# Kernel tuning notes

Measured on AMD Instinct MI355X. Metric: run time of the kernel, lower is better.

Reference implementation:

```python
import jax, jax.numpy as jnp
import numpy as np

B, T, D, H = 8, 1024, 1024, 16
HD = D // H
SCALE = HD ** -0.5


def setup_inputs() -> dict:
    key = jax.random.key(0)
    ks = jax.random.split(key, 5)
    s = 0.02
    return {
        "hidden_states": jax.random.normal(ks[0], (B, T, D), jnp.float32),
        "Wq": jax.random.normal(ks[1], (D, D), jnp.float32) * s,
        "bq": jnp.zeros((D,), jnp.float32),
        "Wk": jax.random.normal(ks[2], (D, D), jnp.float32) * s,
        "bk": jnp.zeros((D,), jnp.float32),
        "Wv": jax.random.normal(ks[3], (D, D), jnp.float32) * s,
        "bv": jnp.zeros((D,), jnp.float32),
        "Wo": jax.random.normal(ks[4], (D, D), jnp.float32) * s,
        "bo": jnp.zeros((D,), jnp.float32),
    }


def _split_heads(x):
    # [B, T, D] -> [B, H, T, HD]
    return x.reshape(B, T, H, HD).transpose(0, 2, 1, 3)


def reference(hidden_states, Wq, bq, Wk, bk, Wv, bv, Wo, bo):
    q = _split_heads((hidden_states @ Wq + bq) * SCALE)
    k = _split_heads(hidden_states @ Wk + bk)
    v = _split_heads(hidden_states @ Wv + bv)
    # [B, H, T, T] attention scores
    scores = jnp.einsum("bhqd,bhkd->bhqk", q, k)
    probs = jax.nn.softmax(scores, axis=-1)
    attn = jnp.einsum("bhqk,bhkd->bhqd", probs, v)
    attn = attn.transpose(0, 2, 1, 3).reshape(B, T, D)
    return attn @ Wo + bo
```

## Files before the change

kernel.cpp:

```cpp
#include <hip/hip_runtime.h>

typedef unsigned short u16;
typedef __attribute__((ext_vector_type(4))) float f32x4;
typedef __attribute__((ext_vector_type(8))) __bf16 bf16x8;
typedef __attribute__((ext_vector_type(4))) __bf16 bf16x4;
typedef __attribute__((ext_vector_type(4))) unsigned short u16x4;
typedef __attribute__((ext_vector_type(8))) unsigned short u16x8;

static __device__ __forceinline__ u16 f2bf(float f) {
    union { float f; unsigned u; } v; v.f = f;
    unsigned r = v.u + 0x7FFFu + ((v.u >> 16) & 1u);
    return (u16)(r >> 16);
}

static __device__ __forceinline__ float exp2f_fast(float x) {
    float r; asm("v_exp_f32 %0, %1" : "=v"(r) : "v"(x)); return r;
}

static __device__ __forceinline__ void gload16(const u16* g, u16* l) {
    __builtin_amdgcn_global_load_lds(
        (const __attribute__((address_space(1))) unsigned int*)g,
        (__attribute__((address_space(3))) unsigned int*)l, 16, 0, 0);
}

template<int N> static __device__ __forceinline__ void vm_wait() {
    if constexpr (N >= 8)      asm volatile("s_waitcnt vmcnt(8)" ::: "memory");
    else if constexpr (N == 6) asm volatile("s_waitcnt vmcnt(6)" ::: "memory");
    else if constexpr (N == 4) asm volatile("s_waitcnt vmcnt(4)" ::: "memory");
    else if constexpr (N == 3) asm volatile("s_waitcnt vmcnt(3)" ::: "memory");
    else                       asm volatile("s_waitcnt vmcnt(0)" ::: "memory");
}

#define SWZ64(row, ec) (((row) * 64) + ((((ec) ^ ((row) & 7))) << 3))

__global__ __launch_bounds__(256) void k_cvt(const float* __restrict__ in, u16* __restrict__ out) {
    size_t i = (size_t)blockIdx.x * 256 + threadIdx.x;
    float4 v = ((const float4*)in)[i];
    u16x4 o; o[0] = f2bf(v.x); o[1] = f2bf(v.y); o[2] = f2bf(v.z); o[3] = f2bf(v.w);
    *(u16x4*)(out + i * 4) = o;
}

__global__ __launch_bounds__(256) void k_wtrans4(
    const float* __restrict__ W0, const float* __restrict__ W1,
    const float* __restrict__ W2, const float* __restrict__ W3,
    u16* __restrict__ T0, u16* __restrict__ T1, u16* __restrict__ T2, u16* __restrict__ T3,
    float s0) {
    const float* W; u16* Tt; float sc;
    switch (blockIdx.z) {
        case 0:  W = W0; Tt = T0; sc = s0;  break;
        case 1:  W = W1; Tt = T1; sc = 1.f; break;
        case 2:  W = W2; Tt = T2; sc = 1.f; break;
        default: W = W3; Tt = T3; sc = 1.f; break;
    }
    __shared__ float tile[32][33];
    int n0 = blockIdx.x * 32, k0 = blockIdx.y * 32;
    int tid = threadIdx.x;
    int r = tid >> 3, c = (tid & 7) * 4;
    float4 v = *(const float4*)(W + (size_t)(k0 + r) * 1024 + n0 + c);
    tile[r][c] = v.x; tile[r][c + 1] = v.y; tile[r][c + 2] = v.z; tile[r][c + 3] = v.w;
    __syncthreads();
    u16x4 o;
    o[0] = f2bf(tile[c][r] * sc);
    o[1] = f2bf(tile[c + 1][r] * sc);
    o[2] = f2bf(tile[c + 2][r] * sc);
    o[3] = f2bf(tile[c + 3][r] * sc);
    *(u16x4*)(Tt + (size_t)(n0 + r) * 1024 + k0 + c) = o;
}

template<int BN>
__global__ __launch_bounds__(512, 2) void k_g256(
    const u16* __restrict__ A, const u16* __restrict__ Bt,
    const float* __restrict__ bias, const float* __restrict__ biasK, float qscale,
    u16* __restrict__ obf, u16* __restrict__ obK, float* __restrict__ of32,
    int ldc, int bias_row, int nblk, int mode) {
    constexpr int WN = (BN == 256) ? 4 : 2;
    constexpr int WAVE_M = (BN == 256) ? 128 : 64;
    constexpr int M_REP = WAVE_M / 16;
    constexpr int BCALLS = BN / 128;
    constexpr int LPT = 2 + BCALLS;
    constexpr int ASLOT = 256 * 32;
    constexpr int BSLOT = BN * 32;
    __shared__ u16 As[4 * ASLOT];
    __shared__ u16 Bs[4 * BSLOT];
    const int tid = threadIdx.x;
    const int l = tid & 63, w = tid >> 6;
    const int mw = w / WN, nw = w % WN;
    const int fr = l & 15, gg = l >> 4, f4 = gg * 4;
    const int id = blockIdx.x;
    const int swz = (id & 7) * 32 + (id >> 3);
    const int bm = swz / nblk, bn = swz % nblk;
    const size_t m0 = (size_t)bm * 256, n0v = (size_t)bn * BN;

    const int srow = w * 16 + (l >> 2);
    const int schk = ((l & 3) ^ ((l >> 3) & 3)) * 8;
    const u16* agp0 = A + (m0 + srow) * 1024 + schk;
    const u16* agp1 = A + (m0 + 128 + srow) * 1024 + schk;
    const u16* bgp0 = Bt + (n0v + srow) * 1024 + schk;
    const u16* bgp1 = (BN == 256) ? Bt + (n0v + 128 + srow) * 1024 + schk : bgp0;
    const int ldst = w * 512 + l * 8;

    const int fchk = (gg ^ ((fr >> 1) & 3)) * 8;
    int aoff[8], boff[4];
#pragma unroll
    for (int mt = 0; mt < 8; ++mt) aoff[mt] = (mw * WAVE_M + mt * 16 + fr) * 32 + fchk;
#pragma unroll
    for (int nt = 0; nt < 4; ++nt) boff[nt] = (nw * 64 + nt * 16 + fr) * 32 + fchk;

    f32x4 acc[8][4] = {};

#define PSTG(S, J)                                                              \
    gload16(agp0 + (size_t)(J) * 32, As + (S) * ASLOT + ldst);                  \
    gload16(agp1 + (size_t)(J) * 32, As + (S) * ASLOT + 4096 + ldst);           \
    gload16(bgp0 + (size_t)(J) * 32, Bs + (S) * BSLOT + ldst);                  \
    if constexpr (BN == 256)                                                    \
        gload16(bgp1 + (size_t)(J) * 32, Bs + (S) * BSLOT + 4096 + ldst);
    PSTG(0, 0) PSTG(1, 1) PSTG(2, 2)
#undef PSTG

#define TILE(S, J, VMN, STG)                                                    \
    {                                                                           \
        vm_wait<VMN>();                                                         \
        __builtin_amdgcn_s_barrier();                                           \
        bf16x8 afr[4], bfr[4];                                                  \
        _Pragma("unroll")                                                       \
        for (int nt = 0; nt < 4; ++nt)                                          \
            bfr[nt] = *(const bf16x8*)(&Bs[(S) * BSLOT + boff[nt]]);            \
        _Pragma("unroll")                                                       \
        for (int mt = 0; mt < 4; ++mt)                                          \
            afr[mt] = *(const bf16x8*)(&As[(S) * ASLOT + aoff[mt]]);            \
        if constexpr (STG) {                                                    \
            gload16(agp0 + (size_t)((J) + 3) * 32, As + (((S) + 3) & 3) * ASLOT + ldst);        \
            gload16(agp1 + (size_t)((J) + 3) * 32, As + (((S) + 3) & 3) * ASLOT + 4096 + ldst); \
            if constexpr (BN == 128)                                            \
                gload16(bgp0 + (size_t)((J) + 3) * 32, Bs + (((S) + 3) & 3) * BSLOT + ldst);    \
        }                                                                       \
        __builtin_amdgcn_s_barrier();                                           \
        asm volatile("s_waitcnt lgkmcnt(0)" ::: "memory");                      \
        __builtin_amdgcn_sched_barrier(0);                                      \
        __builtin_amdgcn_s_setprio(1);                                          \
        _Pragma("unroll")                                                       \
        for (int mt = 0; mt < 4; ++mt)                                          \
            _Pragma("unroll")                                                   \
            for (int nt = 0; nt < 4; ++nt)                                      \
                acc[mt][nt] = __builtin_amdgcn_mfma_f32_16x16x32_bf16(afr[mt], bfr[nt], acc[mt][nt], 0, 0, 0); \
        __builtin_amdgcn_s_setprio(0);                                          \
        if constexpr (BN == 256) {                                              \
            _Pragma("unroll")                                                   \
            for (int mt = 0; mt < 4; ++mt)                                      \
                afr[mt] = *(const bf16x8*)(&As[(S) * ASLOT + aoff[4 + mt]]);    \
            if constexpr (STG) {                                                \
                gload16(bgp0 + (size_t)((J) + 3) * 32, Bs + (((S) + 3) & 3) * BSLOT + ldst);        \
                gload16(bgp1 + (size_t)((J) + 3) * 32, Bs + (((S) + 3) & 3) * BSLOT + 4096 + ldst); \
            }                                                                   \
            __builtin_amdgcn_s_barrier();                                       \
            asm volatile("s_waitcnt lgkmcnt(0)" ::: "memory");                  \
            __builtin_amdgcn_sched_barrier(0);                                  \
            __builtin_amdgcn_s_setprio(1);                                      \
            _Pragma("unroll")                                                   \
            for (int mt = 0; mt < 4; ++mt)                                      \
                _Pragma("unroll")                                               \
                for (int nt = 0; nt < 4; ++nt)                                  \
                    acc[4 + mt][nt] = __builtin_amdgcn_mfma_f32_16x16x32_bf16(afr[mt], bfr[nt], acc[4 + mt][nt], 0, 0, 0); \
            __builtin_amdgcn_s_setprio(0);                                      \
        }                                                                       \
    }

#pragma unroll 1
    for (int jb = 0; jb < 28; jb += 4) {
        TILE(0, jb + 0, (2 * LPT), true)
        TILE(1, jb + 1, (2 * LPT), true)
        TILE(2, jb + 2, (2 * LPT), true)
        TILE(3, jb + 3, (2 * LPT), true)
    }
    TILE(0, 28, (2 * LPT), true)
    TILE(1, 29, (2 * LPT), false)
    TILE(2, 30, LPT, false)
    TILE(3, 31, 0, false)
#undef TILE

    const int mrow0 = (int)m0 + mw * WAVE_M;
    const int ncol0 = (int)n0v + nw * 64;
    if (mode == 1) {
#pragma unroll
        for (int mt = 0; mt < M_REP; ++mt)
#pragma unroll
            for (int nt = 0; nt < 4; ++nt) {
                const int col = ncol0 + nt * 16 + fr;
                const int seg = col >> 10, colm = col & 1023;
                const float bb = (seg ? biasK[colm] : bias[colm] * qscale);
                u16* op = seg ? obK : obf;
#pragma unroll
                for (int r = 0; r < 4; ++r)
                    op[(size_t)(mrow0 + mt * 16 + f4 + r) * 1024 + colm] = f2bf(acc[mt][nt][r] + bb);
            }
    } else if (mode == 2) {
#pragma unroll
        for (int mt = 0; mt < M_REP; ++mt) {
            float rb_[4];
#pragma unroll
            for (int r = 0; r < 4; ++r) rb_[r] = bias[mrow0 + mt * 16 + f4 + r];
#pragma unroll
            for (int nt = 0; nt < 4; ++nt) {
                const int col = ncol0 + nt * 16 + fr;
                const int colp = (col & ~31) | (((col >> 2) & 3) << 3) |
                                 (((col >> 4) & 1) << 2) | (col & 3);
#pragma unroll
                for (int r = 0; r < 4; ++r) {
                    const size_t row = (size_t)(mrow0 + mt * 16 + f4 + r);
                    obf[row * (size_t)ldc + colp] = f2bf(acc[mt][nt][r] + rb_[r]);
                }
            }
        }
    } else {
#pragma unroll
        for (int mt = 0; mt < M_REP; ++mt) {
            float rb_[4];
#pragma unroll
            for (int r = 0; r < 4; ++r)
                rb_[r] = bias_row ? bias[mrow0 + mt * 16 + f4 + r] : 0.f;
#pragma unroll
            for (int nt = 0; nt < 4; ++nt) {
                const int col = ncol0 + nt * 16 + fr;
                const float cb = bias_row ? 0.f : bias[col];
#pragma unroll
                for (int r = 0; r < 4; ++r) {
                    const size_t row = (size_t)(mrow0 + mt * 16 + f4 + r);
                    const float vv = acc[mt][nt][r] + cb + rb_[r];
                    if (of32) of32[row * (size_t)ldc + col] = vv;
                    else      obf[row * (size_t)ldc + col] = f2bf(vv);
                }
            }
        }
    }
}

static __device__ __forceinline__ void qk_tile(const u16* Ks, int fr, int gg,
                                               bf16x8 qA0, bf16x8 qA1, bf16x8 qB0, bf16x8 qB1,
                                               float mA, float mB, f32x4 sA[4], f32x4 sB[4]) {
    __builtin_amdgcn_s_setprio(1);
#pragma unroll
    for (int nt = 0; nt < 4; ++nt) {
        const int rk = nt * 16 + fr;
        const bf16x8 kf0 = *(const bf16x8*)(&Ks[SWZ64(rk, gg)]);
        const bf16x8 kf1 = *(const bf16x8*)(&Ks[SWZ64(rk, gg + 4)]);
        f32x4 z = {-mA, -mA, -mA, -mA};
        z = __builtin_amdgcn_mfma_f32_16x16x32_bf16(kf0, qA0, z, 0, 0, 0);
        z = __builtin_amdgcn_mfma_f32_16x16x32_bf16(kf1, qA1, z, 0, 0, 0);
        sA[nt] = z;
        f32x4 y = {-mB, -mB, -mB, -mB};
        y = __builtin_amdgcn_mfma_f32_16x16x32_bf16(kf0, qB0, y, 0, 0, 0);
        y = __builtin_amdgcn_mfma_f32_16x16x32_bf16(kf1, qB1, y, 0, 0, 0);
        sB[nt] = y;
    }
    __builtin_amdgcn_s_setprio(0);
}

static __device__ __forceinline__ void sm_tile(const f32x4 s[4], f32x4 o[4],
                                               float& m, float& lsum, bf16x4 p[4]) {
    float mymax = s[0][0];
#pragma unroll
    for (int nt = 0; nt < 4; ++nt)
#pragma unroll
        for (int r = 0; r < 4; ++r) mymax = fmaxf(mymax, s[nt][r]);
    float ps = 0.f;
#pragma unroll
    for (int nt = 0; nt < 4; ++nt)
#pragma unroll
        for (int r = 0; r < 4; ++r) {
            const float pp = exp2f_fast(s[nt][r]);
            ps += pp; p[nt][r] = (__bf16)pp;
        }
    if (__builtin_expect(__any(mymax > 11.0f), 0)) {
        float rm = fmaxf(mymax, __shfl_xor(mymax, 16, 64));
        rm = fmaxf(rm, __shfl_xor(rm, 32, 64));
        const float d = fmaxf(rm, 0.f);
        const float fac = exp2f_fast(-d);
        m += d; lsum *= fac;
#pragma unroll
        for (int mt = 0; mt < 4; ++mt)
#pragma unroll
            for (int r = 0; r < 4; ++r) o[mt][r] *= fac;
        ps = 0.f;
#pragma unroll
        for (int nt = 0; nt < 4; ++nt)
#pragma unroll
            for (int r = 0; r < 4; ++r) {
                const float pp = exp2f_fast(s[nt][r] - d);
                ps += pp; p[nt][r] = (__bf16)pp;
            }
    }
    lsum += ps;
}

static __device__ __forceinline__ void pv_tile(const u16* Vs, int fr, int gg,
                                               const bf16x4 pA[4], const bf16x4 pB[4],
                                               f32x4 oA[4], f32x4 oB[4]) {
    const bf16x8 BA0 = __builtin_shufflevector(pA[0], pA[1], 0, 1, 2, 3, 4, 5, 6, 7);
    const bf16x8 BA1 = __builtin_shufflevector(pA[2], pA[3], 0, 1, 2, 3, 4, 5, 6, 7);
    const bf16x8 BB0 = __builtin_shufflevector(pB[0], pB[1], 0, 1, 2, 3, 4, 5, 6, 7);
    const bf16x8 BB1 = __builtin_shufflevector(pB[2], pB[3], 0, 1, 2, 3, 4, 5, 6, 7);
    __builtin_amdgcn_s_setprio(1);
#pragma unroll
    for (int mt = 0; mt < 4; ++mt) {
        const int rv = mt * 16 + fr;
        const bf16x8 vk0 = *(const bf16x8*)(&Vs[SWZ64(rv, gg)]);
        const bf16x8 vk1 = *(const bf16x8*)(&Vs[SWZ64(rv, gg + 4)]);
        oA[mt] = __builtin_amdgcn_mfma_f32_16x16x32_bf16(vk0, BA0, oA[mt], 0, 0, 0);
        oA[mt] = __builtin_amdgcn_mfma_f32_16x16x32_bf16(vk1, BA1, oA[mt], 0, 0, 0);
        oB[mt] = __builtin_amdgcn_mfma_f32_16x16x32_bf16(vk0, BB0, oB[mt], 0, 0, 0);
        oB[mt] = __builtin_amdgcn_mfma_f32_16x16x32_bf16(vk1, BB1, oB[mt], 0, 0, 0);
    }
    __builtin_amdgcn_s_setprio(0);
}

__global__ __launch_bounds__(256, 2) void k_flash(const u16* __restrict__ Q, const u16* __restrict__ K,
                                                  const u16* __restrict__ Vt2, u16* __restrict__ O) {
    __shared__ u16 Ks[4][64 * 64];
    __shared__ u16 Vs[4][64 * 64];
    const int tid = threadIdx.x;
    const int l = tid & 63, w = tid >> 6;
    const int id = blockIdx.x;
    const int swz = (id & 7) * 128 + (id >> 3);
    const int bh = swz >> 3, qt = swz & 7;
    const int b = bh >> 4, h = bh & 15;
    const int qw = qt * 128 + w * 32;
    const int fr = l & 15, gg = l >> 4, f4 = gg * 4, f8 = gg * 8;

    const u16* qpA = Q + ((size_t)(b * 1024 + qw + fr)) * 1024 + h * 64 + f8;
    const u16* qpB = qpA + 16 * 1024;
    const bf16x8 qA0 = *(const bf16x8*)qpA;
    const bf16x8 qA1 = *(const bf16x8*)(qpA + 32);
    const bf16x8 qB0 = *(const bf16x8*)qpB;
    const bf16x8 qB1 = *(const bf16x8*)(qpB + 32);

    const int jj0 = w * 2, jj1 = w * 2 + 1;
    const int sr0 = jj0 * 8 + (l >> 3), sr1 = jj1 * 8 + (l >> 3);
    const int sc = ((l & 7) ^ (l >> 3)) * 8;
    const u16* kg0 = K + ((size_t)(b * 1024 + sr0)) * 1024 + h * 64 + sc;
    const u16* kg1 = K + ((size_t)(b * 1024 + sr1)) * 1024 + h * 64 + sc;
    const u16* vg0 = Vt2 + ((size_t)(h * 64 + sr0)) * 8192 + b * 1024 + sc;
    const u16* vg1 = Vt2 + ((size_t)(h * 64 + sr1)) * 8192 + b * 1024 + sc;
    const int lk0 = jj0 * 512 + l * 8, lk1 = jj1 * 512 + l * 8;

#define FSTG(S, kt)                                         \
    gload16(kg0 + (size_t)(kt) * 1024, Ks[S] + lk0);        \
    gload16(kg1 + (size_t)(kt) * 1024, Ks[S] + lk1);        \
    gload16(vg0 + (kt), Vs[S] + lk0);                       \
    gload16(vg1 + (kt), Vs[S] + lk1);

    f32x4 oA[4] = {}, oB[4] = {};
    float mA = 0.f, lA = 0.f, mB = 0.f, lB = 0.f;
    bf16x4 p0A[4], p0B[4], p1A[4], p1B[4];

    FSTG(0, 0) FSTG(1, 64)

#define FITER(T, PCA, PCB, PPA, PPB, VMN, DOPV)                              \
    {                                                                        \
        vm_wait<VMN>();                                                      \
        __builtin_amdgcn_s_barrier();                                        \
        f32x4 sA[4], sB[4];                                                  \
        qk_tile(Ks[(T) & 3], fr, gg, qA0, qA1, qB0, qB1, mA, mB, sA, sB);    \
        if ((T) + 2 <= 15) { FSTG((((T) + 2) & 3), ((T) + 2) * 64) }         \
        if (DOPV) pv_tile(Vs[((T) - 1) & 3], fr, gg, PPA, PPB, oA, oB);      \
        sm_tile(sA, oA, mA, lA, PCA);                                        \
        sm_tile(sB, oB, mB, lB, PCB);                                        \
    }

    FITER(0,  p0A, p0B, p1A, p1B, 4, false)
    FITER(1,  p1A, p1B, p0A, p0B, 4, true)
    FITER(2,  p0A, p0B, p1A, p1B, 4, true)
    FITER(3,  p1A, p1B, p0A, p0B, 4, true)
    FITER(4,  p0A, p0B, p1A, p1B, 4, true)
    FITER(5,  p1A, p1B, p0A, p0B, 4, true)
    FITER(6,  p0A, p0B, p1A, p1B, 4, true)
    FITER(7,  p1A, p1B, p0A, p0B, 4, true)
    FITER(8,  p0A, p0B, p1A, p1B, 4, true)
    FITER(9,  p1A, p1B, p0A, p0B, 4, true)
    FITER(10, p0A, p0B, p1A, p1B, 4, true)
    FITER(11, p1A, p1B, p0A, p0B, 4, true)
    FITER(12, p0A, p0B, p1A, p1B, 4, true)
    FITER(13, p1A, p1B, p0A, p0B, 4, true)
    FITER(14, p0A, p0B, p1A, p1B, 4, true)
    FITER(15, p1A, p1B, p0A, p0B, 0, true)
#undef FITER
#undef FSTG
    pv_tile(Vs[3], fr, gg, p1A, p1B, oA, oB);

    lA += __shfl_xor(lA, 16, 64); lA += __shfl_xor(lA, 32, 64);
    lB += __shfl_xor(lB, 16, 64); lB += __shfl_xor(lB, 32, 64);
    const float ivA = 1.0f / lA, ivB = 1.0f / lB;
    u16* opA = O + ((size_t)(b * 1024 + qw + fr)) * 1024 + h * 64;
    u16* opB = opA + 16 * 1024;
#pragma unroll
    for (int mt = 0; mt < 4; ++mt) {
        u16x4 oa, ob;
#pragma unroll
        for (int r = 0; r < 4; ++r) { oa[r] = f2bf(oA[mt][r] * ivA); ob[r] = f2bf(oB[mt][r] * ivB); }
        *(u16x4*)(opA + mt * 16 + f4) = oa;
        *(u16x4*)(opB + mt * 16 + f4) = ob;
    }
}

extern "C" void kernel_launch(void* const* d_in, const int* in_sizes, int n_in,
                              void* d_out, int out_size, void* d_ws, size_t ws_size,
                              hipStream_t stream) {
    (void)in_sizes; (void)n_in; (void)out_size; (void)ws_size;
    const float* hs = (const float*)d_in[0];
    const float* Wq = (const float*)d_in[1];
    const float* bq = (const float*)d_in[2];
    const float* Wk = (const float*)d_in[3];
    const float* bk = (const float*)d_in[4];
    const float* Wv = (const float*)d_in[5];
    const float* bv = (const float*)d_in[6];
    const float* Wo = (const float*)d_in[7];
    const float* bo = (const float*)d_in[8];
    float* out = (float*)d_out;
    char* ws = (char*)d_ws;
    const size_t MB = 1024ull * 1024ull;
    u16* Xb  = (u16*)(ws);
    u16* Wqt = (u16*)(ws + 16 * MB);
    u16* Wkt = (u16*)(ws + 18 * MB);
    u16* Wvt = (u16*)(ws + 20 * MB);
    u16* Wot = (u16*)(ws + 22 * MB);
    u16* Qb  = (u16*)(ws + 24 * MB);
    u16* Kb  = (u16*)(ws + 40 * MB);
    u16* Vt2 = (u16*)(ws + 56 * MB);
    u16* Ob  = Xb;

    const float SCALE_Q = 0.125f * 1.4426950408889634f;

    k_cvt<<<dim3(8192), dim3(256), 0, stream>>>(hs, Xb);
    k_wtrans4<<<dim3(32, 32, 4), dim3(256), 0, stream>>>(Wq, Wk, Wv, Wo, Wqt, Wkt, Wvt, Wot, SCALE_Q);
    k_g256<256><<<dim3(256), dim3(512), 0, stream>>>(Xb, Wqt, bq, bk, SCALE_Q,
                                                     Qb, Kb, nullptr, 1024, 0, 8, 1);
    k_g256<128><<<dim3(256), dim3(512), 0, stream>>>(Wvt, Xb, bv, nullptr, 1.f,
                                                     Vt2, nullptr, nullptr, 8192, 1, 64, 2);
    k_flash<<<dim3(1024), dim3(256), 0, stream>>>(Qb, Kb, Vt2, Ob);
    k_g256<128><<<dim3(256), dim3(512), 0, stream>>>(Ob, Wot, bo, nullptr, 1.f,
                                                     nullptr, nullptr, out, 1024, 0, 8, 0);
}
```

Measured before the change: 150.8 us.

## Restructure GEMM mainloop to double-buffered BK=64 tiles with phased prefetch

Replaces the 4-stage BK=32 LDS ring with a 2-stage BK=64 double buffer. Each K tile is split into phases whose global-to-LDS loads for the next tile are interleaved between MFMA groups, and the LDS swizzle is changed to an 8-chunk XOR pattern. The aim is fewer barriers and wait points per unit of K and less per-iteration overhead. In exchange there is shallower prefetch depth, since each tile waits on vmcnt(0), which may expose more global load latency.

```diff
diff --git a/kernel.cpp b/kernel.cpp
--- a/kernel.cpp
+++ b/kernel.cpp
@@ -76,12 +76,10 @@
     constexpr int WN = (BN == 256) ? 4 : 2;
     constexpr int WAVE_M = (BN == 256) ? 128 : 64;
     constexpr int M_REP = WAVE_M / 16;
-    constexpr int BCALLS = BN / 128;
-    constexpr int LPT = 2 + BCALLS;
-    constexpr int ASLOT = 256 * 32;
-    constexpr int BSLOT = BN * 32;
-    __shared__ u16 As[4 * ASLOT];
-    __shared__ u16 Bs[4 * BSLOT];
+    constexpr int ABUF = 256 * 64;
+    constexpr int BBUF = BN * 64;
+    __shared__ u16 As[2 * ABUF];
+    __shared__ u16 Bs[2 * BBUF];
     const int tid = threadIdx.x;
     const int l = tid & 63, w = tid >> 6;
     const int mw = w / WN, nw = w % WN;
@@ -91,92 +89,104 @@
     const int bm = swz / nblk, bn = swz % nblk;
     const size_t m0 = (size_t)bm * 256, n0v = (size_t)bn * BN;
 
-    const int srow = w * 16 + (l >> 2);
-    const int schk = ((l & 3) ^ ((l >> 3) & 3)) * 8;
-    const u16* agp0 = A + (m0 + srow) * 1024 + schk;
-    const u16* agp1 = A + (m0 + 128 + srow) * 1024 + schk;
-    const u16* bgp0 = Bt + (n0v + srow) * 1024 + schk;
-    const u16* bgp1 = (BN == 256) ? Bt + (n0v + 128 + srow) * 1024 + schk : bgp0;
-    const int ldst = w * 512 + l * 8;
-
-    const int fchk = (gg ^ ((fr >> 1) & 3)) * 8;
-    int aoff[8], boff[4];
-#pragma unroll
-    for (int mt = 0; mt < 8; ++mt) aoff[mt] = (mw * WAVE_M + mt * 16 + fr) * 32 + fchk;
-#pragma unroll
-    for (int nt = 0; nt < 4; ++nt) boff[nt] = (nw * 64 + nt * 16 + fr) * 32 + fchk;
-
-    f32x4 acc[8][4] = {};
-
-#define PSTG(S, J)                                                              \
-    gload16(agp0 + (size_t)(J) * 32, As + (S) * ASLOT + ldst);                  \
-    gload16(agp1 + (size_t)(J) * 32, As + (S) * ASLOT + 4096 + ldst);           \
-    gload16(bgp0 + (size_t)(J) * 32, Bs + (S) * BSLOT + ldst);                  \
-    if constexpr (BN == 256)                                                    \
-        gload16(bgp1 + (size_t)(J) * 32, Bs + (S) * BSLOT + 4096 + ldst);
-    PSTG(0, 0) PSTG(1, 1) PSTG(2, 2)
-#undef PSTG
-
-#define TILE(S, J, VMN, STG)                                                    \
-    {                                                                           \
-        vm_wait<VMN>();                                                         \
-        __builtin_amdgcn_s_barrier();                                           \
-        bf16x8 afr[4], bfr[4];                                                  \
-        _Pragma("unroll")                                                       \
-        for (int nt = 0; nt < 4; ++nt)                                          \
-            bfr[nt] = *(const bf16x8*)(&Bs[(S) * BSLOT + boff[nt]]);            \
-        _Pragma("unroll")                                                       \
-        for (int mt = 0; mt < 4; ++mt)                                          \
-            afr[mt] = *(const bf16x8*)(&As[(S) * ASLOT + aoff[mt]]);            \
-        if constexpr (STG) {                                                    \
-            gload16(agp0 + (size_t)((J) + 3) * 32, As + (((S) + 3) & 3) * ASLOT + ldst);        \
-            gload16(agp1 + (size_t)((J) + 3) * 32, As + (((S) + 3) & 3) * ASLOT + 4096 + ldst); \
-            if constexpr (BN == 128)                                            \
-                gload16(bgp0 + (size_t)((J) + 3) * 32, Bs + (((S) + 3) & 3) * BSLOT + ldst);    \
-        }                                                                       \
-        __builtin_amdgcn_s_barrier();                                           \
-        asm volatile("s_waitcnt lgkmcnt(0)" ::: "memory");                      \
-        __builtin_amdgcn_sched_barrier(0);                                      \
-        __builtin_amdgcn_s_setprio(1);                                          \
-        _Pragma("unroll")                                                       \
-        for (int mt = 0; mt < 4; ++mt)                                          \
-            _Pragma("unroll")                                                   \
-            for (int nt = 0; nt < 4; ++nt)                                      \
-                acc[mt][nt] = __builtin_amdgcn_mfma_f32_16x16x32_bf16(afr[mt], bfr[nt], acc[mt][nt], 0, 0, 0); \
-        __builtin_amdgcn_s_setprio(0);                                          \
-        if constexpr (BN == 256) {                                              \
-            _Pragma("unroll")                                                   \
-            for (int mt = 0; mt < 4; ++mt)                                      \
-                afr[mt] = *(const bf16x8*)(&As[(S) * ASLOT + aoff[4 + mt]]);    \
-            if constexpr (STG) {                                                \
-                gload16(bgp0 + (size_t)((J) + 3) * 32, Bs + (((S) + 3) & 3) * BSLOT + ldst);        \
-                gload16(bgp1 + (size_t)((J) + 3) * 32, Bs + (((S) + 3) & 3) * BSLOT + 4096 + ldst); \
-            }                                                                   \
-            __builtin_amdgcn_s_barrier();                                       \
-            asm volatile("s_waitcnt lgkmcnt(0)" ::: "memory");                  \
-            __builtin_amdgcn_sched_barrier(0);                                  \
-            __builtin_amdgcn_s_setprio(1);                                      \
-            _Pragma("unroll")                                                   \
-            for (int mt = 0; mt < 4; ++mt)                                      \
-                _Pragma("unroll")                                               \
-                for (int nt = 0; nt < 4; ++nt)                                  \
-                    acc[4 + mt][nt] = __builtin_amdgcn_mfma_f32_16x16x32_bf16(afr[mt], bfr[nt], acc[4 + mt][nt], 0, 0, 0); \
-            __builtin_amdgcn_s_setprio(0);                                      \
-        }                                                                       \
-    }
-
+    const int strow = tid >> 3;
+    const int sch = ((tid & 7) ^ (strow & 7)) * 8;
+    const u16* Ag = A + (m0 + strow) * 1024 + sch;
+    const u16* Bg = Bt + (n0v + strow) * 1024 + sch;
+    const int ldst = tid * 8;
+
+    const int kc0 = (gg ^ (fr & 7)) << 3;
+    const int abase = (mw * WAVE_M + fr) * 64;
+    const int bbase = (nw * 64 + fr) * 64;
+
+    f32x4 acc[M_REP][4] = {};
+
+#define SA(c, J, b) gload16(Ag + (size_t)(c) * 65536 + (size_t)(J) * 64, As + (b) * ABUF + (c) * 4096 + ldst);
+#define SB(c, J, b) gload16(Bg + (size_t)(c) * 65536 + (size_t)(J) * 64, Bs + (b) * BBUF + (c) * 4096 + ldst);
+#define PH_BAR()                                                        \
+    __builtin_amdgcn_s_barrier();                                       \
+    asm volatile("s_waitcnt lgkmcnt(0)" ::: "memory");                  \
+    __builtin_amdgcn_sched_barrier(0)
+#define MFMA16(AB)                                                      \
+    __builtin_amdgcn_s_setprio(1);                                      \
+    _Pragma("unroll")                                                   \
+    for (int mt = 0; mt < 4; ++mt)                                      \
+        _Pragma("unroll")                                               \
+        for (int nt = 0; nt < 4; ++nt)                                  \
+            acc[(AB) + mt][nt] = __builtin_amdgcn_mfma_f32_16x16x32_bf16(afr[mt], bfr[nt], acc[(AB) + mt][nt], 0, 0, 0); \
+    __builtin_amdgcn_s_setprio(0)
+
+    SA(0, 0, 0) SA(1, 0, 0) SA(2, 0, 0) SA(3, 0, 0)
+    SB(0, 0, 0) SB(1, 0, 0)
+    if constexpr (BN == 256) { SB(2, 0, 0) SB(3, 0, 0) }
+
+#define GT256(b, J, STG)                                                                      \
+    {                                                                                         \
+        asm volatile("s_waitcnt vmcnt(0)" ::: "memory");                                      \
+        __builtin_amdgcn_s_barrier();                                                         \
+        bf16x8 bfr[4], afr[4];                                                                \
+        _Pragma("unroll")                                                                     \
+        for (int nt = 0; nt < 4; ++nt) bfr[nt] = *(const bf16x8*)(&Bs[(b) * BBUF + bbase + nt * 1024 + kc0]); \
+        _Pragma("unroll")                                                                     \
+        for (int mt = 0; mt < 4; ++mt) afr[mt] = *(const bf16x8*)(&As[(b) * ABUF + abase + mt * 1024 + kc0]); \
+        if (STG) { SA(0, (J) + 1, (b) ^ 1) SA(1, (J) + 1, (b) ^ 1) }                          \
+        PH_BAR();                                                                             \
+        MFMA16(0);                                                                            \
+        _Pragma("unroll")                                                                     \
+        for (int mt = 0; mt < 4; ++mt) afr[mt] = *(const bf16x8*)(&As[(b) * ABUF + abase + (mt + 4) * 1024 + kc0]); \
+        if (STG) { SA(2, (J) + 1, (b) ^ 1) SA(3, (J) + 1, (b) ^ 1) }                          \
+        PH_BAR();                                                                             \
+        MFMA16(4);                                                                            \
+        _Pragma("unroll")                                                                     \
+        for (int nt = 0; nt < 4; ++nt) bfr[nt] = *(const bf16x8*)(&Bs[(b) * BBUF + bbase + nt * 1024 + (kc0 ^ 32)]); \
+        _Pragma("unroll")                                                                     \
+        for (int mt = 0; mt < 4; ++mt) afr[mt] = *(const bf16x8*)(&As[(b) * ABUF + abase + mt * 1024 + (kc0 ^ 32)]); \
+        if (STG) { SB(0, (J) + 1, (b) ^ 1) SB(1, (J) + 1, (b) ^ 1) }                          \
+        PH_BAR();                                                                             \
+        MFMA16(0);                                                                            \
+        _Pragma("unroll")                                                                     \
+        for (int mt = 0; mt < 4; ++mt) afr[mt] = *(const bf16x8*)(&As[(b) * ABUF + abase + (mt + 4) * 1024 + (kc0 ^ 32)]); \
+        if (STG) { SB(2, (J) + 1, (b) ^ 1) SB(3, (J) + 1, (b) ^ 1) }                          \
+        PH_BAR();                                                                             \
+        MFMA16(4);                                                                            \
+    }
+
+#define GT128(b, J, STG)                                                                      \
+    {                                                                                         \
+        asm volatile("s_waitcnt vmcnt(0)" ::: "memory");                                      \
+        __builtin_amdgcn_s_barrier();                                                         \
+        bf16x8 bfr[4], afr[4];                                                                \
+        _Pragma("unroll")                                                                     \
+        for (int nt = 0; nt < 4; ++nt) bfr[nt] = *(const bf16x8*)(&Bs[(b) * BBUF + bbase + nt * 1024 + kc0]); \
+        _Pragma("unroll")                                                                     \
+        for (int mt = 0; mt < 4; ++mt) afr[mt] = *(const bf16x8*)(&As[(b) * ABUF + abase + mt * 1024 + kc0]); \
+        if (STG) { SA(0, (J) + 1, (b) ^ 1) SA(1, (J) + 1, (b) ^ 1) SB(0, (J) + 1, (b) ^ 1) }  \
+        PH_BAR();                                                                             \
+        MFMA16(0);                                                                            \
+        _Pragma("unroll")                                                                     \
+        for (int nt = 0; nt < 4; ++nt) bfr[nt] = *(const bf16x8*)(&Bs[(b) * BBUF + bbase + nt * 1024 + (kc0 ^ 32)]); \
+        _Pragma("unroll")                                                                     \
+        for (int mt = 0; mt < 4; ++mt) afr[mt] = *(const bf16x8*)(&As[(b) * ABUF + abase + mt * 1024 + (kc0 ^ 32)]); \
+        if (STG) { SA(2, (J) + 1, (b) ^ 1) SA(3, (J) + 1, (b) ^ 1) SB(1, (J) + 1, (b) ^ 1) }  \
+        PH_BAR();                                                                             \
+        MFMA16(0);                                                                            \
+    }
+
+    if constexpr (BN == 256) {
 #pragma unroll 1
-    for (int jb = 0; jb < 28; jb += 4) {
-        TILE(0, jb + 0, (2 * LPT), true)
-        TILE(1, jb + 1, (2 * LPT), true)
-        TILE(2, jb + 2, (2 * LPT), true)
-        TILE(3, jb + 3, (2 * LPT), true)
-    }
-    TILE(0, 28, (2 * LPT), true)
-    TILE(1, 29, (2 * LPT), false)
-    TILE(2, 30, LPT, false)
-    TILE(3, 31, 0, false)
-#undef TILE
+        for (int j = 0; j < 14; j += 2) { GT256(0, j, 1) GT256(1, j + 1, 1) }
+        GT256(0, 14, 1) GT256(1, 15, 0)
+    } else {
+#pragma unroll 1
+        for (int j = 0; j < 14; j += 2) { GT128(0, j, 1) GT128(1, j + 1, 1) }
+        GT128(0, 14, 1) GT128(1, 15, 0)
+    }
+#undef GT256
+#undef GT128
+#undef SA
+#undef SB
+#undef PH_BAR
+#undef MFMA16
 
     const int mrow0 = (int)m0 + mw * WAVE_M;
     const int ncol0 = (int)n0v + nw * 64;
```

After: 153.7 us. Within noise of the previous version (+2.0%).

## Fuse prep kernels and shrink flash attention LDS ring to 2K/3V buffers

Applied to the files above, without the earlier changes.

Merges the input bf16 conversion and the weight transpose into one launch with a flat grid, removing one kernel launch. The flash attention kernel now prefetches one tile ahead into 2 K buffers and 3 V buffers instead of two tiles ahead into 4+4 buffers. That cuts LDS per block, which may allow more resident blocks. The cost is a shorter prefetch distance, so load latency is less hidden and waits are tighter.

```diff
diff --git a/kernel.cpp b/kernel.cpp
--- a/kernel.cpp
+++ b/kernel.cpp
@@ -28,33 +28,38 @@
     else if constexpr (N == 6) asm volatile("s_waitcnt vmcnt(6)" ::: "memory");
     else if constexpr (N == 4) asm volatile("s_waitcnt vmcnt(4)" ::: "memory");
     else if constexpr (N == 3) asm volatile("s_waitcnt vmcnt(3)" ::: "memory");
+    else if constexpr (N == 2) asm volatile("s_waitcnt vmcnt(2)" ::: "memory");
     else                       asm volatile("s_waitcnt vmcnt(0)" ::: "memory");
 }
 
 #define SWZ64(row, ec) (((row) * 64) + ((((ec) ^ ((row) & 7))) << 3))
 
-__global__ __launch_bounds__(256) void k_cvt(const float* __restrict__ in, u16* __restrict__ out) {
-    size_t i = (size_t)blockIdx.x * 256 + threadIdx.x;
-    float4 v = ((const float4*)in)[i];
-    u16x4 o; o[0] = f2bf(v.x); o[1] = f2bf(v.y); o[2] = f2bf(v.z); o[3] = f2bf(v.w);
-    *(u16x4*)(out + i * 4) = o;
-}
-
-__global__ __launch_bounds__(256) void k_wtrans4(
+__global__ __launch_bounds__(256) void k_prep(
+    const float* __restrict__ hs, u16* __restrict__ Xb,
     const float* __restrict__ W0, const float* __restrict__ W1,
     const float* __restrict__ W2, const float* __restrict__ W3,
     u16* __restrict__ T0, u16* __restrict__ T1, u16* __restrict__ T2, u16* __restrict__ T3,
     float s0) {
+    __shared__ float tile[32][33];
+    const int id = blockIdx.x;
+    const int tid = threadIdx.x;
+    if (id < 8192) {
+        size_t i = (size_t)id * 256 + tid;
+        float4 v = ((const float4*)hs)[i];
+        u16x4 o; o[0] = f2bf(v.x); o[1] = f2bf(v.y); o[2] = f2bf(v.z); o[3] = f2bf(v.w);
+        *(u16x4*)(Xb + i * 4) = o;
+        return;
+    }
+    const int wid = id - 8192;
+    const int z = wid >> 10, rem = wid & 1023;
+    const int n0 = (rem & 31) * 32, k0 = (rem >> 5) * 32;
     const float* W; u16* Tt; float sc;
-    switch (blockIdx.z) {
+    switch (z) {
         case 0:  W = W0; Tt = T0; sc = s0;  break;
         case 1:  W = W1; Tt = T1; sc = 1.f; break;
         case 2:  W = W2; Tt = T2; sc = 1.f; break;
         default: W = W3; Tt = T3; sc = 1.f; break;
     }
-    __shared__ float tile[32][33];
-    int n0 = blockIdx.x * 32, k0 = blockIdx.y * 32;
-    int tid = threadIdx.x;
     int r = tid >> 3, c = (tid & 7) * 4;
     float4 v = *(const float4*)(W + (size_t)(k0 + r) * 1024 + n0 + c);
     tile[r][c] = v.x; tile[r][c + 1] = v.y; tile[r][c + 2] = v.z; tile[r][c + 3] = v.w;
@@ -315,8 +320,8 @@
 
 __global__ __launch_bounds__(256, 2) void k_flash(const u16* __restrict__ Q, const u16* __restrict__ K,
                                                   const u16* __restrict__ Vt2, u16* __restrict__ O) {
-    __shared__ u16 Ks[4][64 * 64];
-    __shared__ u16 Vs[4][64 * 64];
+    __shared__ u16 Ks[2][64 * 64];
+    __shared__ u16 Vs[3][64 * 64];
     const int tid = threadIdx.x;
     const int l = tid & 63, w = tid >> 6;
     const int id = blockIdx.x;
@@ -342,9 +347,10 @@
     const u16* vg1 = Vt2 + ((size_t)(h * 64 + sr1)) * 8192 + b * 1024 + sc;
     const int lk0 = jj0 * 512 + l * 8, lk1 = jj1 * 512 + l * 8;
 
-#define FSTG(S, kt)                                         \
+#define FSTGK(S, kt)                                        \
     gload16(kg0 + (size_t)(kt) * 1024, Ks[S] + lk0);        \
-    gload16(kg1 + (size_t)(kt) * 1024, Ks[S] + lk1);        \
+    gload16(kg1 + (size_t)(kt) * 1024, Ks[S] + lk1);
+#define FSTGV(S, kt)                                        \
     gload16(vg0 + (kt), Vs[S] + lk0);                       \
     gload16(vg1 + (kt), Vs[S] + lk1);
 
@@ -352,39 +358,42 @@
     float mA = 0.f, lA = 0.f, mB = 0.f, lB = 0.f;
     bf16x4 p0A[4], p0B[4], p1A[4], p1B[4];
 
-    FSTG(0, 0) FSTG(1, 64)
-
-#define FITER(T, PCA, PCB, PPA, PPB, VMN, DOPV)                              \
+    FSTGK(0, 0) FSTGV(0, 0)
+
+#define FITER(T, QS, PS, KS, VS, PCA, PCB, PPA, PPB, DOPV, DOSTG)            \
     {                                                                        \
-        vm_wait<VMN>();                                                      \
+        vm_wait<2>();                                                        \
         __builtin_amdgcn_s_barrier();                                        \
         f32x4 sA[4], sB[4];                                                  \
-        qk_tile(Ks[(T) & 3], fr, gg, qA0, qA1, qB0, qB1, mA, mB, sA, sB);    \
-        if ((T) + 2 <= 15) { FSTG((((T) + 2) & 3), ((T) + 2) * 64) }         \
-        if (DOPV) pv_tile(Vs[((T) - 1) & 3], fr, gg, PPA, PPB, oA, oB);      \
+        qk_tile(Ks[QS], fr, gg, qA0, qA1, qB0, qB1, mA, mB, sA, sB);         \
+        if (DOSTG) { FSTGK(KS, ((T) + 1) * 64) FSTGV(VS, ((T) + 1) * 64) }   \
+        if (DOPV) pv_tile(Vs[PS], fr, gg, PPA, PPB, oA, oB);                 \
         sm_tile(sA, oA, mA, lA, PCA);                                        \
         sm_tile(sB, oB, mB, lB, PCB);                                        \
     }
 
-    FITER(0,  p0A, p0B, p1A, p1B, 4, false)
-    FITER(1,  p1A, p1B, p0A, p0B, 4, true)
-    FITER(2,  p0A, p0B, p1A, p1B, 4, true)
-    FITER(3,  p1A, p1B, p0A, p0B, 4, true)
-    FITER(4,  p0A, p0B, p1A, p1B, 4, true)
-    FITER(5,  p1A, p1B, p0A, p0B, 4, true)
-    FITER(6,  p0A, p0B, p1A, p1B, 4, true)
-    FITER(7,  p1A, p1B, p0A, p0B, 4, true)
-    FITER(8,  p0A, p0B, p1A, p1B, 4, true)
-    FITER(9,  p1A, p1B, p0A, p0B, 4, true)
-    FITER(10, p0A, p0B, p1A, p1B, 4, true)
-    FITER(11, p1A, p1B, p0A, p0B, 4, true)
-    FITER(12, p0A, p0B, p1A, p1B, 4, true)
-    FITER(13, p1A, p1B, p0A, p0B, 4, true)
-    FITER(14, p0A, p0B, p1A, p1B, 4, true)
-    FITER(15, p1A, p1B, p0A, p0B, 0, true)
+    FITER(0,  0, 0, 1, 1, p0A, p0B, p1A, p1B, 0, 1)
+    FITER(1,  1, 0, 0, 2, p1A, p1B, p0A, p0B, 1, 1)
+    FITER(2,  0, 1, 1, 0, p0A, p0B, p1A, p1B, 1, 1)
+    FITER(3,  1, 2, 0, 1, p1A, p1B, p0A, p0B, 1, 1)
+    FITER(4,  0, 0, 1, 2, p0A, p0B, p1A, p1B, 1, 1)
+    FITER(5,  1, 1, 0, 0, p1A, p1B, p0A, p0B, 1, 1)
+    FITER(6,  0, 2, 1, 1, p0A, p0B, p1A, p1B, 1, 1)
+    FITER(7,  1, 0, 0, 2, p1A, p1B, p0A, p0B, 1, 1)
+    FITER(8,  0, 1, 1, 0, p0A, p0B, p1A, p1B, 1, 1)
+    FITER(9,  1, 2, 0, 1, p1A, p1B, p0A, p0B, 1, 1)
+    FITER(10, 0, 0, 1, 2, p0A, p0B, p1A, p1B, 1, 1)
+    FITER(11, 1, 1, 0, 0, p1A, p1B, p0A, p0B, 1, 1)
+    FITER(12, 0, 2, 1, 1, p0A, p0B, p1A, p1B, 1, 1)
+    FITER(13, 1, 0, 0, 2, p1A, p1B, p0A, p0B, 1, 1)
+    FITER(14, 0, 1, 1, 0, p0A, p0B, p1A, p1B, 1, 1)
+    FITER(15, 1, 2, 0, 0, p1A, p1B, p0A, p0B, 1, 0)
 #undef FITER
-#undef FSTG
-    pv_tile(Vs[3], fr, gg, p1A, p1B, oA, oB);
+    vm_wait<0>();
+    __builtin_amdgcn_s_barrier();
+    pv_tile(Vs[0], fr, gg, p1A, p1B, oA, oB);
+#undef FSTGK
+#undef FSTGV
 
     lA += __shfl_xor(lA, 16, 64); lA += __shfl_xor(lA, 32, 64);
     lB += __shfl_xor(lB, 16, 64); lB += __shfl_xor(lB, 32, 64);
@@ -429,8 +438,8 @@
 
     const float SCALE_Q = 0.125f * 1.4426950408889634f;
 
-    k_cvt<<<dim3(8192), dim3(256), 0, stream>>>(hs, Xb);
-    k_wtrans4<<<dim3(32, 32, 4), dim3(256), 0, stream>>>(Wq, Wk, Wv, Wo, Wqt, Wkt, Wvt, Wot, SCALE_Q);
+    k_prep<<<dim3(12288), dim3(256), 0, stream>>>(hs, Xb, Wq, Wk, Wv, Wo,
+                                                  Wqt, Wkt, Wvt, Wot, SCALE_Q);
     k_g256<256><<<dim3(256), dim3(512), 0, stream>>>(Xb, Wqt, bq, bk, SCALE_Q,
                                                      Qb, Kb, nullptr, 1024, 0, 8, 1);
     k_g256<128><<<dim3(256), dim3(512), 0, stream>>>(Wvt, Xb, bv, nullptr, 1.f,
```

New measurement: 145.7 us, median of 2. 3.3% less time.
